# Optimization experiments

Hardware: AMD Instinct MI355X
Metric: run time of the kernel (lower is better)

The kernel has to match this reference:

```python
import jax, jax.numpy as jnp
import numpy as np

EPS = 1e-5  # BatchNorm eps


def _spmm(x, src, dst, dinv, n):
    # normalized adjacency SpMM: out[d] = dinv[d] * sum_{(s,d) in E} dinv[s] * x[s]
    msg = x[src] * dinv[src][:, None]                      # [E, d]
    agg = jax.ops.segment_sum(msg, dst, num_segments=n)   # [N, d]
    return agg * dinv[:, None]


def _cheb(x, W, b, src, dst, dinv, n):
    # Chebyshev recursion with lambda_max=2: Lhat = -Ahat
    # T0 = X, T1 = Lhat X, Tk = 2 Lhat T_{k-1} - T_{k-2}; out = sum_k T_k W_k + b
    X0 = x
    X1 = -_spmm(x, src, dst, dinv, n)
    out = X0 @ W[0] + X1 @ W[1]
    Xp, Xc = X0, X1
    for k in range(2, W.shape[0]):
        Xn = -2.0 * _spmm(Xc, src, dst, dinv, n) - Xp
        out = out + Xn @ W[k]
        Xp, Xc = Xc, Xn
    return out + b


def _bn(x, gamma, beta):
    # BatchNorm1d over nodes (training-mode batch stats)
    mu = jnp.mean(x, axis=0)
    var = jnp.var(x, axis=0)
    return (x - mu) * jax.lax.rsqrt(var + EPS) * gamma + beta


def setup_inputs() -> dict:
    key = jax.random.key(0)
    ks = jax.random.split(key, 8)
    n, e, fin, h, fout, K = 50000, 800000, 128, 128, 64, 3
    def w(k, shape, fan_in):
        return jax.random.normal(k, shape, jnp.float32) * np.float32(1.0 / np.sqrt(fan_in))
    return {
        "features": jax.random.normal(ks[0], (n, fin), jnp.float32),
        "src": jax.random.randint(ks[1], (e,), 0, n),
        "dst": jax.random.randint(ks[2], (e,), 0, n),
        "W1": w(ks[3], (K, fin, h), K * fin), "b1": jnp.zeros((h,), jnp.float32),
        "W2": w(ks[4], (K, h, h), K * h), "b2": jnp.zeros((h,), jnp.float32),
        "W3": w(ks[5], (K, h, h), K * h), "b3": jnp.zeros((h,), jnp.float32),
        "gamma": jnp.ones((h,), jnp.float32), "beta": jnp.zeros((h,), jnp.float32),
        "mw1": w(ks[6], (h, h), h), "mb1": jnp.zeros((h,), jnp.float32),
        "mw2": w(ks[7], (h, fout), h), "mb2": jnp.zeros((fout,), jnp.float32),
    }


def reference(features, src, dst, W1, b1, W2, b2, W3, b3, gamma, beta, mw1, mb1, mw2, mb2):
    n = features.shape[0]
    deg = jax.ops.segment_sum(jnp.ones(dst.shape, features.dtype), dst, num_segments=n)
    dinv = jax.lax.rsqrt(jnp.maximum(deg, 1.0))
    x = jax.nn.relu(_cheb(features, W1, b1, src, dst, dinv, n))
    x = _bn(x, gamma, beta)
    for _ in range(1, 3):  # self.k = 3 -> cheb2 applied twice (shared weights)
        x = jax.nn.relu(_cheb(x, W2, b2, src, dst, dinv, n))
    x_res = x
    x = jax.nn.relu(_cheb(x, W3, b3, src, dst, dinv, n))
    x = x + x_res  # dropout treated as identity (eval mode)
    return jax.nn.relu(x @ mw1 + mb1) @ mw2 + mb2
```

## Files before the change

kernel.cpp:

```cpp
#include <hip/hip_runtime.h>
#include <hip/hip_bf16.h>

typedef __attribute__((ext_vector_type(4))) float f32x4;
typedef __attribute__((ext_vector_type(8))) short short8;

__device__ inline unsigned short f2bf(float f) {
    union { float f; unsigned int u; } v; v.f = f;
    unsigned int u = v.u;
    return (unsigned short)((u + 0x7fffu + ((u >> 16) & 1u)) >> 16);
}
__device__ inline float bf2f(unsigned short h) {
    union { unsigned int u; float f; } v; v.u = ((unsigned int)h) << 16; return v.f;
}
__device__ inline float bflo(unsigned int p) {
    union { unsigned int u; float f; } v; v.u = p << 16; return v.f;
}
__device__ inline float bfhi(unsigned int p) {
    union { unsigned int u; float f; } v; v.u = p & 0xffff0000u; return v.f;
}
__device__ inline unsigned int packbf(float a, float b) {
    return (unsigned int)f2bf(a) | ((unsigned int)f2bf(b) << 16);
}

#define EPT 4096


__global__ __launch_bounds__(256) void cast_k(const float* __restrict__ x, unsigned short* __restrict__ y, int n4) {
    int i = blockIdx.x * 256 + threadIdx.x;
    if (i >= n4) return;
    f32x4 v = ((const f32x4*)x)[i];
    uint2 o; o.x = packbf(v[0], v[1]); o.y = packbf(v[2], v[3]);
    ((uint2*)y)[i] = o;
}


__global__ __launch_bounds__(256) void deg_rank_k(const int* __restrict__ dst, int* __restrict__ deg,
                                                  int* __restrict__ rank, int e) {
    int i = blockIdx.x * 256 + threadIdx.x;
    if (i < e) rank[i] = atomicAdd(&deg[dst[i]], 1);
}

__global__ __launch_bounds__(256) void partial_k(const int* __restrict__ deg, int* __restrict__ part, int n) {
    __shared__ int sm[256];
    int t = threadIdx.x;
    int base = blockIdx.x * 1024 + t * 4;
    int s = 0;
#pragma unroll
    for (int j = 0; j < 4; ++j) { int idx = base + j; if (idx < n) s += deg[idx]; }
    sm[t] = s;
    __syncthreads();
    for (int off = 128; off > 0; off >>= 1) {
        if (t < off) sm[t] += sm[t + off];
        __syncthreads();
    }
    if (t == 0) part[blockIdx.x] = sm[0];
}

__global__ __launch_bounds__(256) void scanpart_k(int* __restrict__ part, int nb) {
    __shared__ int sm[256];
    int t = threadIdx.x;
    int v = (t < nb) ? part[t] : 0;
    sm[t] = v;
    __syncthreads();
    for (int off = 1; off < 256; off <<= 1) {
        int u = (t >= off) ? sm[t - off] : 0;
        __syncthreads();
        sm[t] += u;
        __syncthreads();
    }
    if (t < nb) part[t] = sm[t] - v;
}

__global__ __launch_bounds__(256) void rowptr_k(const int* __restrict__ deg, const int* __restrict__ part,
                                                int* __restrict__ rowptr, float* __restrict__ dinv, int n) {
    __shared__ int sm[256];
    int t = threadIdx.x;
    int base = blockIdx.x * 1024 + t * 4;
    int d[4]; int s = 0;
#pragma unroll
    for (int j = 0; j < 4; ++j) { int idx = base + j; d[j] = (idx < n) ? deg[idx] : 0; s += d[j]; }
    sm[t] = s;
    __syncthreads();
    for (int off = 1; off < 256; off <<= 1) {
        int u = (t >= off) ? sm[t - off] : 0;
        __syncthreads();
        sm[t] += u;
        __syncthreads();
    }
    int ex = part[blockIdx.x] + sm[t] - s;
#pragma unroll
    for (int j = 0; j < 4; ++j) {
        int idx = base + j;
        if (idx < n) {
            rowptr[idx] = ex;
            dinv[idx] = rsqrtf(fmaxf((float)d[j], 1.0f));
        }
        ex += d[j];
    }
    if (blockIdx.x == gridDim.x - 1 && t == 255) rowptr[n] = part[blockIdx.x] + sm[255];
}

__global__ __launch_bounds__(256) void scatter8r_k(const int* __restrict__ src, const int* __restrict__ dst,
                                                   const int* __restrict__ rowptr, const int* __restrict__ rank,
                                                   int* __restrict__ csrc, int e, int n, int n8) {
    int r = blockIdx.x & 7;
    int chunk = blockIdx.x >> 3;
    int base = chunk * EPT;
    int lim = base + EPT; if (lim > e) lim = e;
    int lo = r * n8;
    int hi = lo + n8; if (hi > n) hi = n;
    for (int i = base + threadIdx.x; i < lim; i += 256) {
        int d = dst[i];
        if (d >= lo && d < hi) {
            csrc[rowptr[d] + rank[i]] = src[i];
        }
    }
}


template<bool AFF>
__global__ __launch_bounds__(256) void spmm_bf_k(const unsigned short* __restrict__ x, const int* __restrict__ rowptr,
                                                 const int* __restrict__ csrc, const float* __restrict__ dinv,
                                                 const float* __restrict__ gscale, const float* __restrict__ goff,
                                                 unsigned short* __restrict__ out, int n) {
    int lane = threadIdx.x & 63;
    int wave = threadIdx.x >> 6;
    int node = blockIdx.x * 4 + wave;
    if (node >= n) return;
    int g = lane >> 4;
    int c = lane & 15;
    int beg = rowptr[node], end = rowptr[node + 1];
    float acc[8];
    float sw = 0.f;
#pragma unroll
    for (int j = 0; j < 8; ++j) acc[j] = 0.f;

    int i = beg + g;
    for (; i + 12 < end; i += 16) {
        int s0 = csrc[i], s1 = csrc[i + 4], s2 = csrc[i + 8], s3 = csrc[i + 12];
        float w0 = dinv[s0], w1 = dinv[s1], w2 = dinv[s2], w3 = dinv[s3];
        uint4 v0 = ((const uint4*)(x + (size_t)s0 * 128))[c];
        uint4 v1 = ((const uint4*)(x + (size_t)s1 * 128))[c];
        uint4 v2 = ((const uint4*)(x + (size_t)s2 * 128))[c];
        uint4 v3 = ((const uint4*)(x + (size_t)s3 * 128))[c];
        if (AFF) sw += w0 + w1 + w2 + w3;
        acc[0] += w0 * bflo(v0.x); acc[1] += w0 * bfhi(v0.x);
        acc[2] += w0 * bflo(v0.y); acc[3] += w0 * bfhi(v0.y);
        acc[4] += w0 * bflo(v0.z); acc[5] += w0 * bfhi(v0.z);
        acc[6] += w0 * bflo(v0.w); acc[7] += w0 * bfhi(v0.w);
        acc[0] += w1 * bflo(v1.x); acc[1] += w1 * bfhi(v1.x);
        acc[2] += w1 * bflo(v1.y); acc[3] += w1 * bfhi(v1.y);
        acc[4] += w1 * bflo(v1.z); acc[5] += w1 * bfhi(v1.z);
        acc[6] += w1 * bflo(v1.w); acc[7] += w1 * bfhi(v1.w);
        acc[0] += w2 * bflo(v2.x); acc[1] += w2 * bfhi(v2.x);
        acc[2] += w2 * bflo(v2.y); acc[3] += w2 * bfhi(v2.y);
        acc[4] += w2 * bflo(v2.z); acc[5] += w2 * bfhi(v2.z);
        acc[6] += w2 * bflo(v2.w); acc[7] += w2 * bfhi(v2.w);
        acc[0] += w3 * bflo(v3.x); acc[1] += w3 * bfhi(v3.x);
        acc[2] += w3 * bflo(v3.y); acc[3] += w3 * bfhi(v3.y);
        acc[4] += w3 * bflo(v3.z); acc[5] += w3 * bfhi(v3.z);
        acc[6] += w3 * bflo(v3.w); acc[7] += w3 * bfhi(v3.w);
    }
    for (; i < end; i += 4) {
        int s0 = csrc[i];
        float w0 = dinv[s0];
        uint4 v0 = ((const uint4*)(x + (size_t)s0 * 128))[c];
        if (AFF) sw += w0;
        acc[0] += w0 * bflo(v0.x); acc[1] += w0 * bfhi(v0.x);
        acc[2] += w0 * bflo(v0.y); acc[3] += w0 * bfhi(v0.y);
        acc[4] += w0 * bflo(v0.z); acc[5] += w0 * bfhi(v0.z);
        acc[6] += w0 * bflo(v0.w); acc[7] += w0 * bfhi(v0.w);
    }

#pragma unroll
    for (int j = 0; j < 8; ++j) {
        acc[j] += __shfl_xor(acc[j], 16, 64);
        acc[j] += __shfl_xor(acc[j], 32, 64);
    }
    if (AFF) {
        sw += __shfl_xor(sw, 16, 64);
        sw += __shfl_xor(sw, 32, 64);
    }

    float dd = dinv[node];
    if (g == 0) {
        if (AFF) {
            f32x4 sc0 = ((const f32x4*)(gscale + c * 8))[0];
            f32x4 sc1 = ((const f32x4*)(gscale + c * 8))[1];
            f32x4 of0 = ((const f32x4*)(goff + c * 8))[0];
            f32x4 of1 = ((const f32x4*)(goff + c * 8))[1];
#pragma unroll
            for (int j = 0; j < 4; ++j) {
                acc[j] = sc0[j] * acc[j] + of0[j] * sw;
                acc[4 + j] = sc1[j] * acc[4 + j] + of1[j] * sw;
            }
        }
        uint4 o;
        o.x = packbf(acc[0] * dd, acc[1] * dd);
        o.y = packbf(acc[2] * dd, acc[3] * dd);
        o.z = packbf(acc[4] * dd, acc[5] * dd);
        o.w = packbf(acc[6] * dd, acc[7] * dd);
        ((uint4*)(out + (size_t)node * 128))[c] = o;
    }
}


__device__ inline void pack_one(const float* __restrict__ W, unsigned short* __restrict__ out,
                                int K, int N, int cheb, int id) {
    int total = (K / 32) * (N / 16) * 64;
    if (id >= total) return;
    int lane = id & 63;
    int t2 = id >> 6;
    int nf = N / 16;
    int f = t2 % nf;
    int ks = t2 / nf;
    int col = f * 16 + (lane & 15);
    int kbase = ks * 32 + ((lane >> 4) * 8);
    for (int j = 0; j < 8; ++j) {
        int kg = kbase + j;
        float v;
        if (cheb) {
            int t = kg >> 7, kk = kg & 127;
            float w0 = W[kk * 128 + col], wb = W[16384 + kk * 128 + col], wc = W[32768 + kk * 128 + col];
            v = (t == 0) ? (w0 - wc) : (t == 1) ? (-wb) : (2.0f * wc);
        } else {
            v = W[(size_t)kg * N + col];
        }
        out[(size_t)id * 8 + j] = f2bf(v);
    }
}

__global__ __launch_bounds__(256) void pack_all_k(const float* W1, unsigned short* wp1,
                                                  const float* W2, unsigned short* wp2,
                                                  const float* W3, unsigned short* wp3,
                                                  const float* mw1, unsigned short* wpm1,
                                                  const float* mw2, unsigned short* wpm2) {
    int b = blockIdx.x, t = threadIdx.x;
    if (b < 24)       pack_one(W1, wp1, 384, 128, 1, b * 256 + t);
    else if (b < 48)  pack_one(W2, wp2, 384, 128, 1, (b - 24) * 256 + t);
    else if (b < 72)  pack_one(W3, wp3, 384, 128, 1, (b - 48) * 256 + t);
    else if (b < 80)  pack_one(mw1, wpm1, 128, 128, 0, (b - 72) * 256 + t);
    else              pack_one(mw2, wpm2, 128, 64, 0, (b - 80) * 256 + t);
}


__global__ __launch_bounds__(128) void bn_coef_k(const float* __restrict__ gsum, const float* __restrict__ gsqs,
                                                 const float* __restrict__ gamma, const float* __restrict__ beta,
                                                 float* __restrict__ gscale, float* __restrict__ goff, float inv_n) {
    int c = threadIdx.x;
    float mu = gsum[c] * inv_n;
    float var = gsqs[c] * inv_n - mu * mu;
    float sc = rsqrtf(var + 1e-5f) * gamma[c];
    gscale[c] = sc;
    goff[c] = beta[c] - mu * sc;
}


template<bool RELU, bool RES, bool STATS, bool AFFA, bool MLP>
__global__ __launch_bounds__(512, 4) void gemm_k(const unsigned short* __restrict__ s0,
                                                 const unsigned short* __restrict__ s1,
                                                 const unsigned short* __restrict__ s2,
                                                 const unsigned short* __restrict__ wp,
                                                 const float* __restrict__ bias,
                                                 const unsigned short* __restrict__ resid,
                                                 const float* __restrict__ gscale,
                                                 const float* __restrict__ goff,
                                                 float* __restrict__ gsum, float* __restrict__ gsqs,
                                                 unsigned short* __restrict__ outp,
                                                 const unsigned short* __restrict__ wpm1,
                                                 const float* __restrict__ mb1,
                                                 const unsigned short* __restrict__ wpm2,
                                                 const float* __restrict__ mb2,
                                                 float* __restrict__ outf, int n) {
    __shared__ char blds[49152];
    __shared__ char tl[MLP ? 32768 : 16];
    __shared__ float bs[STATS ? 128 : 1], bq[STATS ? 128 : 1];
    int t = threadIdx.x;
    int lane = t & 63;
    int wave = t >> 6;
    int row0 = blockIdx.x * 128;

    if (STATS && t < 128) { bs[t] = 0.f; bq[t] = 0.f; }

    int rowA = row0 + wave * 16 + (lane & 15);
    if (rowA >= n) rowA = n - 1;
    int kg = (lane >> 4) * 8;
    int colb = lane & 15;

    {
        const char* gsrc = (const char*)wp;
        int wbase = wave * 6144;
#pragma unroll
        for (int j = 0; j < 6; ++j) {
            int off = wbase + j * 1024;
            __builtin_amdgcn_global_load_lds((const unsigned int*)(gsrc + off + lane * 16),
                                             (unsigned int*)(blds + off), 16, 0, 0);
        }
    }

    short8 a[12];
#pragma unroll
    for (int ks = 0; ks < 12; ++ks) {
        const unsigned short* sp = (ks < 4) ? s0 : ((ks < 8) ? s1 : s2);
        int kk = (ks & 3) * 32 + kg;
        a[ks] = *(const short8*)(sp + (size_t)rowA * 128 + kk);
    }
    if (AFFA) {
#pragma unroll
        for (int ks = 0; ks < 4; ++ks) {
            int kk = ks * 32 + kg;
            union { unsigned short u[8]; short8 v; } af;
#pragma unroll
            for (int j = 0; j < 8; ++j) {
                float xv = bf2f((unsigned short)a[ks][j]);
                af.u[j] = f2bf(xv * gscale[kk + j] + goff[kk + j]);
            }
            a[ks] = af.v;
        }
    }
#pragma unroll
    for (int ks = 0; ks < 12; ++ks) {
        f32x4 kv = *(f32x4*)&a[ks];
        asm volatile("" :: "v"(kv));
    }

    f32x4 acc[8];
#pragma unroll
    for (int f = 0; f < 8; ++f) acc[f] = (f32x4)(0.0f);

#pragma unroll
    for (int half = 0; half < 2; ++half) {
        __syncthreads();

#pragma unroll
        for (int ks6 = 0; ks6 < 6; ++ks6) {
            int ks = half * 6 + ks6;
#pragma unroll
            for (int f = 0; f < 8; ++f) {
                short8 bb = *(const short8*)(blds + (ks6 * 8 + f) * 1024 + lane * 16);
                acc[f] = __builtin_amdgcn_mfma_f32_16x16x32_bf16(a[ks], bb, acc[f], 0, 0, 0);
            }
        }

        if (half == 0) {
            __syncthreads();
            const char* gsrc = (const char*)wp + 49152;
            int wbase = wave * 6144;
#pragma unroll
            for (int j = 0; j < 6; ++j) {
                int off = wbase + j * 1024;
                __builtin_amdgcn_global_load_lds((const unsigned int*)(gsrc + off + lane * 16),
                                                 (unsigned int*)(blds + off), 16, 0, 0);
            }
        }
    }

    int rowD = row0 + wave * 16 + ((lane >> 4) << 2);
    int lrowD = wave * 16 + ((lane >> 4) << 2);
#pragma unroll
    for (int f = 0; f < 8; ++f) {
        int c = f * 16 + colb;
        float bv = bias[c];
        float ls = 0.f, lq = 0.f;
#pragma unroll
        for (int r = 0; r < 4; ++r) {
            int row = rowD + r;
            if (row >= n) continue;
            float v = acc[f][r] + bv;
            if (RELU) v = fmaxf(v, 0.0f);
            if (RES) v += bf2f(resid[(size_t)row * 128 + c]);
            if (STATS) { ls += v; lq += v * v; }
            if (MLP) {
                int lrow = lrowD + r;
                int byte = lrow * 256 + c * 2;
                byte ^= ((lrow & 7) << 4);
                *(unsigned short*)(tl + byte) = f2bf(v);
            } else {
                outp[(size_t)row * 128 + c] = f2bf(v);
            }
        }
        if (STATS) { atomicAdd(&bs[c], ls); atomicAdd(&bq[c], lq); }
    }

    if (STATS) {
        __syncthreads();
        if (t < 128) {
            atomicAdd(&gsum[t], bs[t]);
            atomicAdd(&gsqs[t], bq[t]);
        }
    }

    if (MLP) {
        __syncthreads();
        {
            int wbase = wave * 6144;
#pragma unroll
            for (int j = 0; j < 6; ++j) {
                int off = wbase + j * 1024;
                const char* g = (off < 32768) ? ((const char*)wpm1 + off)
                                              : ((const char*)wpm2 + (off - 32768));
                __builtin_amdgcn_global_load_lds((const unsigned int*)(g + lane * 16),
                                                 (unsigned int*)(blds + off), 16, 0, 0);
            }
        }
        __syncthreads();

        int lrowA = wave * 16 + (lane & 15);
        f32x4 acc2[8];
#pragma unroll
        for (int f = 0; f < 8; ++f) acc2[f] = (f32x4)(0.0f);
#pragma unroll
        for (int ks = 0; ks < 4; ++ks) {
            int byte = lrowA * 256 + (ks * 32 + kg) * 2;
            byte ^= ((lrowA & 7) << 4);
            short8 av = *(const short8*)(tl + byte);
#pragma unroll
            for (int f = 0; f < 8; ++f) {
                short8 b = *(const short8*)(blds + (ks * 8 + f) * 1024 + lane * 16);
                acc2[f] = __builtin_amdgcn_mfma_f32_16x16x32_bf16(av, b, acc2[f], 0, 0, 0);
            }
        }
        __syncthreads();

#pragma unroll
        for (int f = 0; f < 8; ++f) {
            int c = f * 16 + colb;
            float bv = mb1[c];
#pragma unroll
            for (int r = 0; r < 4; ++r) {
                int lrow = lrowD + r;
                float v = fmaxf(acc2[f][r] + bv, 0.0f);
                int byte = lrow * 256 + c * 2;
                byte ^= ((lrow & 7) << 4);
                *(unsigned short*)(tl + byte) = f2bf(v);
            }
        }
        __syncthreads();

        f32x4 acc3[4];
#pragma unroll
        for (int f = 0; f < 4; ++f) acc3[f] = (f32x4)(0.0f);
#pragma unroll
        for (int ks = 0; ks < 4; ++ks) {
            int byte = lrowA * 256 + (ks * 32 + kg) * 2;
            byte ^= ((lrowA & 7) << 4);
            short8 av = *(const short8*)(tl + byte);
#pragma unroll
            for (int f = 0; f < 4; ++f) {
                short8 b = *(const short8*)(blds + 32768 + (ks * 4 + f) * 1024 + lane * 16);
                acc3[f] = __builtin_amdgcn_mfma_f32_16x16x32_bf16(av, b, acc3[f], 0, 0, 0);
            }
        }
#pragma unroll
        for (int f = 0; f < 4; ++f) {
            int c = f * 16 + colb;
            float bv = mb2[c];
#pragma unroll
            for (int r = 0; r < 4; ++r) {
                int row = rowD + r;
                if (row >= n) continue;
                outf[(size_t)row * 64 + c] = acc3[f][r] + bv;
            }
        }
    }
}


extern "C" void kernel_launch(void* const* d_in, const int* in_sizes, int n_in,
                              void* d_out, int out_size, void* d_ws, size_t ws_size,
                              hipStream_t stream) {
    const float* feat  = (const float*)d_in[0];
    const int*   src   = (const int*)d_in[1];
    const int*   dst   = (const int*)d_in[2];
    const float* W1    = (const float*)d_in[3];
    const float* b1    = (const float*)d_in[4];
    const float* W2    = (const float*)d_in[5];
    const float* b2    = (const float*)d_in[6];
    const float* W3    = (const float*)d_in[7];
    const float* b3    = (const float*)d_in[8];
    const float* gamma = (const float*)d_in[9];
    const float* beta  = (const float*)d_in[10];
    const float* mw1   = (const float*)d_in[11];
    const float* mb1   = (const float*)d_in[12];
    const float* mw2   = (const float*)d_in[13];
    const float* mb2   = (const float*)d_in[14];
    float* outp = (float*)d_out;

    const int n = in_sizes[0] / 128;
    const int e = in_sizes[1];
    const int n8 = (n + 7) / 8;

    char* w = (char*)d_ws;
    auto alloc = [&](size_t bytes) -> void* {
        void* p = (void*)w;
        w += (bytes + 255) & ~(size_t)255;
        return p;
    };
    unsigned short* featb = (unsigned short*)alloc((size_t)n * 128 * 2);
    unsigned short* buf0  = (unsigned short*)alloc((size_t)n * 128 * 2);
    unsigned short* buf1  = (unsigned short*)alloc((size_t)n * 128 * 2);
    unsigned short* buf2  = (unsigned short*)alloc((size_t)n * 128 * 2);
    unsigned short* buf3  = (unsigned short*)alloc((size_t)n * 128 * 2);
    int*   deg    = (int*)alloc((size_t)n * 4);
    float* dinv   = (float*)alloc((size_t)n * 4);
    int*   rowptr = (int*)alloc((size_t)(n + 1) * 4);
    int*   rank   = (int*)alloc((size_t)e * 4);
    int*   csrc   = (int*)alloc((size_t)e * 4);
    int*   part   = (int*)alloc(256 * 4);
    unsigned short* wp1  = (unsigned short*)alloc(12 * 8 * 512 * 2);
    unsigned short* wp2  = (unsigned short*)alloc(12 * 8 * 512 * 2);
    unsigned short* wp3  = (unsigned short*)alloc(12 * 8 * 512 * 2);
    unsigned short* wpm1 = (unsigned short*)alloc(4 * 8 * 512 * 2);
    unsigned short* wpm2 = (unsigned short*)alloc(4 * 4 * 512 * 2);
    float* gsum   = (float*)alloc(128 * 4);
    float* gsqs   = (float*)alloc(128 * 4);
    float* gscale = (float*)alloc(128 * 4);
    float* goff   = (float*)alloc(128 * 4);

    const int gGemm = (n + 127) / 128;
    const int gSpmm = (n + 3) / 4;
    const int nb = (n + 1023) / 1024;
    const int gE  = (e + 255) / 256;
    const int gE8 = 8 * ((e + EPT - 1) / EPT);

    cast_k<<<(n * 32 + 255) / 256, 256, 0, stream>>>(feat, featb, n * 32);
    hipMemsetAsync(deg, 0, (size_t)n * 4, stream);
    hipMemsetAsync(gsum, 0, 1024, stream);
    deg_rank_k<<<gE, 256, 0, stream>>>(dst, deg, rank, e);
    partial_k<<<nb, 256, 0, stream>>>(deg, part, n);
    scanpart_k<<<1, 256, 0, stream>>>(part, nb);
    rowptr_k<<<nb, 256, 0, stream>>>(deg, part, rowptr, dinv, n);
    scatter8r_k<<<gE8, 256, 0, stream>>>(src, dst, rowptr, rank, csrc, e, n, n8);
    pack_all_k<<<84, 256, 0, stream>>>(W1, wp1, W2, wp2, W3, wp3, mw1, wpm1, mw2, wpm2);

    spmm_bf_k<false><<<gSpmm, 256, 0, stream>>>(featb, rowptr, csrc, dinv, nullptr, nullptr, buf1, n);
    spmm_bf_k<false><<<gSpmm, 256, 0, stream>>>(buf1, rowptr, csrc, dinv, nullptr, nullptr, buf2, n);
    gemm_k<true, false, true, false, false><<<gGemm, 512, 0, stream>>>(
        featb, buf1, buf2, wp1, b1, nullptr, nullptr, nullptr, gsum, gsqs, buf0,
        nullptr, nullptr, nullptr, nullptr, nullptr, n);
    bn_coef_k<<<1, 128, 0, stream>>>(gsum, gsqs, gamma, beta, gscale, goff, 1.0f / (float)n);

    spmm_bf_k<true><<<gSpmm, 256, 0, stream>>>(buf0, rowptr, csrc, dinv, gscale, goff, buf1, n);
    spmm_bf_k<false><<<gSpmm, 256, 0, stream>>>(buf1, rowptr, csrc, dinv, nullptr, nullptr, buf2, n);
    gemm_k<true, false, false, true, false><<<gGemm, 512, 0, stream>>>(
        buf0, buf1, buf2, wp2, b2, nullptr, gscale, goff, nullptr, nullptr, buf3,
        nullptr, nullptr, nullptr, nullptr, nullptr, n);

    spmm_bf_k<false><<<gSpmm, 256, 0, stream>>>(buf3, rowptr, csrc, dinv, nullptr, nullptr, buf1, n);
    spmm_bf_k<false><<<gSpmm, 256, 0, stream>>>(buf1, rowptr, csrc, dinv, nullptr, nullptr, buf2, n);
    gemm_k<true, false, false, false, false><<<gGemm, 512, 0, stream>>>(
        buf3, buf1, buf2, wp2, b2, nullptr, nullptr, nullptr, nullptr, nullptr, buf0,
        nullptr, nullptr, nullptr, nullptr, nullptr, n);

    spmm_bf_k<false><<<gSpmm, 256, 0, stream>>>(buf0, rowptr, csrc, dinv, nullptr, nullptr, buf1, n);
    spmm_bf_k<false><<<gSpmm, 256, 0, stream>>>(buf1, rowptr, csrc, dinv, nullptr, nullptr, buf2, n);
    gemm_k<true, true, false, false, true><<<gGemm, 512, 0, stream>>>(
        buf0, buf1, buf2, wp3, b3, buf0, nullptr, nullptr, nullptr, nullptr, nullptr,
        wpm1, mb1, wpm2, mb2, outp, n);
}
```

Baseline: 433.8 us.

## Fuse second Chebyshev SpMM into GEMM kernel with T2 staged in LDS

The separate second SpMM launch of each Chebyshev layer is replaced by a fused spgemm kernel. In it, each block of 64 rows first gathers its neighbors' T1 rows via CSR, writes the aggregated T2 tile as bf16 into swizzled LDS, and then runs the MFMA GEMM over T0, T1 and the LDS-resident T2. This removes four kernel launches and the global write and re-read of the T2 intermediate buffer. In exchange, blocks shrink to 256 threads and 64 rows, A operands are loaded per k-step instead of kept in registers, and LDS use per block grows. The serial per-wave gather may also be latency-bound at the reduced occupancy.

```diff
diff --git a/kernel.cpp b/kernel.cpp
--- a/kernel.cpp
+++ b/kernel.cpp
@@ -257,71 +257,111 @@
 
 
 template<bool RELU, bool RES, bool STATS, bool AFFA, bool MLP>
-__global__ __launch_bounds__(512, 4) void gemm_k(const unsigned short* __restrict__ s0,
-                                                 const unsigned short* __restrict__ s1,
-                                                 const unsigned short* __restrict__ s2,
-                                                 const unsigned short* __restrict__ wp,
-                                                 const float* __restrict__ bias,
-                                                 const unsigned short* __restrict__ resid,
-                                                 const float* __restrict__ gscale,
-                                                 const float* __restrict__ goff,
-                                                 float* __restrict__ gsum, float* __restrict__ gsqs,
-                                                 unsigned short* __restrict__ outp,
-                                                 const unsigned short* __restrict__ wpm1,
-                                                 const float* __restrict__ mb1,
-                                                 const unsigned short* __restrict__ wpm2,
-                                                 const float* __restrict__ mb2,
-                                                 float* __restrict__ outf, int n) {
+__global__ __launch_bounds__(256, 4) void spgemm_k(const unsigned short* __restrict__ s0,
+                                                   const unsigned short* __restrict__ s1,
+                                                   const int* __restrict__ rowptr,
+                                                   const int* __restrict__ csrc,
+                                                   const float* __restrict__ dinv,
+                                                   const unsigned short* __restrict__ wp,
+                                                   const float* __restrict__ bias,
+                                                   const unsigned short* __restrict__ resid,
+                                                   const float* __restrict__ gscale,
+                                                   const float* __restrict__ goff,
+                                                   float* __restrict__ gsum, float* __restrict__ gsqs,
+                                                   unsigned short* __restrict__ outp,
+                                                   const unsigned short* __restrict__ wpm1,
+                                                   const float* __restrict__ mb1,
+                                                   const unsigned short* __restrict__ wpm2,
+                                                   const float* __restrict__ mb2,
+                                                   float* __restrict__ outf, int n) {
     __shared__ char blds[49152];
-    __shared__ char tl[MLP ? 32768 : 16];
+    __shared__ char t2l[16384];
     __shared__ float bs[STATS ? 128 : 1], bq[STATS ? 128 : 1];
     int t = threadIdx.x;
     int lane = t & 63;
     int wave = t >> 6;
-    int row0 = blockIdx.x * 128;
+    int row0 = blockIdx.x * 64;
 
     if (STATS && t < 128) { bs[t] = 0.f; bq[t] = 0.f; }
 
-    int rowA = row0 + wave * 16 + (lane & 15);
-    if (rowA >= n) rowA = n - 1;
     int kg = (lane >> 4) * 8;
     int colb = lane & 15;
+    int lrow = wave * 16 + (lane & 15);
+    int rowA = row0 + lrow;
+    if (rowA >= n) rowA = n - 1;
 
     {
         const char* gsrc = (const char*)wp;
-        int wbase = wave * 6144;
-#pragma unroll
-        for (int j = 0; j < 6; ++j) {
+        int wbase = wave * 12288;
+#pragma unroll
+        for (int j = 0; j < 12; ++j) {
             int off = wbase + j * 1024;
             __builtin_amdgcn_global_load_lds((const unsigned int*)(gsrc + off + lane * 16),
                                              (unsigned int*)(blds + off), 16, 0, 0);
         }
     }
 
-    short8 a[12];
-#pragma unroll
-    for (int ks = 0; ks < 12; ++ks) {
-        const unsigned short* sp = (ks < 4) ? s0 : ((ks < 8) ? s1 : s2);
-        int kk = (ks & 3) * 32 + kg;
-        a[ks] = *(const short8*)(sp + (size_t)rowA * 128 + kk);
-    }
-    if (AFFA) {
-#pragma unroll
-        for (int ks = 0; ks < 4; ++ks) {
-            int kk = ks * 32 + kg;
-            union { unsigned short u[8]; short8 v; } af;
+    {
+        int g = lane >> 4;
+        int c = lane & 15;
+        for (int k2 = 0; k2 < 16; ++k2) {
+            int lr = wave * 16 + k2;
+            int node = row0 + lr;
+            if (node >= n) node = n - 1;
+            int beg = rowptr[node], end = rowptr[node + 1];
+            float acc[8];
+#pragma unroll
+            for (int j = 0; j < 8; ++j) acc[j] = 0.f;
+            int i = beg + g;
+            for (; i + 12 < end; i += 16) {
+                int a0 = csrc[i], a1 = csrc[i + 4], a2 = csrc[i + 8], a3 = csrc[i + 12];
+                float w0 = dinv[a0], w1 = dinv[a1], w2 = dinv[a2], w3 = dinv[a3];
+                uint4 v0 = ((const uint4*)(s1 + (size_t)a0 * 128))[c];
+                uint4 v1 = ((const uint4*)(s1 + (size_t)a1 * 128))[c];
+                uint4 v2 = ((const uint4*)(s1 + (size_t)a2 * 128))[c];
+                uint4 v3 = ((const uint4*)(s1 + (size_t)a3 * 128))[c];
+                acc[0] += w0 * bflo(v0.x); acc[1] += w0 * bfhi(v0.x);
+                acc[2] += w0 * bflo(v0.y); acc[3] += w0 * bfhi(v0.y);
+                acc[4] += w0 * bflo(v0.z); acc[5] += w0 * bfhi(v0.z);
+                acc[6] += w0 * bflo(v0.w); acc[7] += w0 * bfhi(v0.w);
+                acc[0] += w1 * bflo(v1.x); acc[1] += w1 * bfhi(v1.x);
+                acc[2] += w1 * bflo(v1.y); acc[3] += w1 * bfhi(v1.y);
+                acc[4] += w1 * bflo(v1.z); acc[5] += w1 * bfhi(v1.z);
+                acc[6] += w1 * bflo(v1.w); acc[7] += w1 * bfhi(v1.w);
+                acc[0] += w2 * bflo(v2.x); acc[1] += w2 * bfhi(v2.x);
+                acc[2] += w2 * bflo(v2.y); acc[3] += w2 * bfhi(v2.y);
+                acc[4] += w2 * bflo(v2.z); acc[5] += w2 * bfhi(v2.z);
+                acc[6] += w2 * bflo(v2.w); acc[7] += w2 * bfhi(v2.w);
+                acc[0] += w3 * bflo(v3.x); acc[1] += w3 * bfhi(v3.x);
+                acc[2] += w3 * bflo(v3.y); acc[3] += w3 * bfhi(v3.y);
+                acc[4] += w3 * bflo(v3.z); acc[5] += w3 * bfhi(v3.z);
+                acc[6] += w3 * bflo(v3.w); acc[7] += w3 * bfhi(v3.w);
+            }
+            for (; i < end; i += 4) {
+                int a0 = csrc[i];
+                float w0 = dinv[a0];
+                uint4 v0 = ((const uint4*)(s1 + (size_t)a0 * 128))[c];
+                acc[0] += w0 * bflo(v0.x); acc[1] += w0 * bfhi(v0.x);
+                acc[2] += w0 * bflo(v0.y); acc[3] += w0 * bfhi(v0.y);
+                acc[4] += w0 * bflo(v0.z); acc[5] += w0 * bfhi(v0.z);
+                acc[6] += w0 * bflo(v0.w); acc[7] += w0 * bfhi(v0.w);
+            }
 #pragma unroll
             for (int j = 0; j < 8; ++j) {
-                float xv = bf2f((unsigned short)a[ks][j]);
-                af.u[j] = f2bf(xv * gscale[kk + j] + goff[kk + j]);
-            }
-            a[ks] = af.v;
-        }
-    }
-#pragma unroll
-    for (int ks = 0; ks < 12; ++ks) {
-        f32x4 kv = *(f32x4*)&a[ks];
-        asm volatile("" :: "v"(kv));
+                acc[j] += __shfl_xor(acc[j], 16, 64);
+                acc[j] += __shfl_xor(acc[j], 32, 64);
+            }
+            float dd = dinv[node];
+            if (g == 0) {
+                uint4 o;
+                o.x = packbf(acc[0] * dd, acc[1] * dd);
+                o.y = packbf(acc[2] * dd, acc[3] * dd);
+                o.z = packbf(acc[4] * dd, acc[5] * dd);
+                o.w = packbf(acc[6] * dd, acc[7] * dd);
+                int byte = (lr * 256 + c * 16) ^ ((lr & 7) << 4);
+                *(uint4*)(t2l + byte) = o;
+            }
+        }
     }
 
     f32x4 acc[8];
@@ -335,19 +375,38 @@
 #pragma unroll
         for (int ks6 = 0; ks6 < 6; ++ks6) {
             int ks = half * 6 + ks6;
+            short8 a;
+            if (ks < 4) {
+                int kk = ks * 32 + kg;
+                a = *(const short8*)(s0 + (size_t)rowA * 128 + kk);
+                if (AFFA) {
+                    union { unsigned short u[8]; short8 v; } af;
+#pragma unroll
+                    for (int j = 0; j < 8; ++j) {
+                        float xv = bf2f((unsigned short)a[j]);
+                        af.u[j] = f2bf(xv * gscale[kk + j] + goff[kk + j]);
+                    }
+                    a = af.v;
+                }
+            } else if (ks < 8) {
+                a = *(const short8*)(s1 + (size_t)rowA * 128 + (ks & 3) * 32 + kg);
+            } else {
+                int byte = (lrow * 256 + ((ks & 3) * 32 + kg) * 2) ^ ((lrow & 7) << 4);
+                a = *(const short8*)(t2l + byte);
+            }
 #pragma unroll
             for (int f = 0; f < 8; ++f) {
                 short8 bb = *(const short8*)(blds + (ks6 * 8 + f) * 1024 + lane * 16);
-                acc[f] = __builtin_amdgcn_mfma_f32_16x16x32_bf16(a[ks], bb, acc[f], 0, 0, 0);
+                acc[f] = __builtin_amdgcn_mfma_f32_16x16x32_bf16(a, bb, acc[f], 0, 0, 0);
             }
         }
 
         if (half == 0) {
             __syncthreads();
             const char* gsrc = (const char*)wp + 49152;
-            int wbase = wave * 6144;
-#pragma unroll
-            for (int j = 0; j < 6; ++j) {
+            int wbase = wave * 12288;
+#pragma unroll
+            for (int j = 0; j < 12; ++j) {
                 int off = wbase + j * 1024;
                 __builtin_amdgcn_global_load_lds((const unsigned int*)(gsrc + off + lane * 16),
                                                  (unsigned int*)(blds + off), 16, 0, 0);
@@ -371,10 +430,9 @@
             if (RES) v += bf2f(resid[(size_t)row * 128 + c]);
             if (STATS) { ls += v; lq += v * v; }
             if (MLP) {
-                int lrow = lrowD + r;
-                int byte = lrow * 256 + c * 2;
-                byte ^= ((lrow & 7) << 4);
-                *(unsigned short*)(tl + byte) = f2bf(v);
+                int lrw = lrowD + r;
+                int byte = (lrw * 256 + c * 2) ^ ((lrw & 7) << 4);
+                *(unsigned short*)(t2l + byte) = f2bf(v);
             } else {
                 outp[(size_t)row * 128 + c] = f2bf(v);
             }
@@ -393,9 +451,9 @@
     if (MLP) {
         __syncthreads();
         {
-            int wbase = wave * 6144;
-#pragma unroll
-            for (int j = 0; j < 6; ++j) {
+            int wbase = wave * 12288;
+#pragma unroll
+            for (int j = 0; j < 12; ++j) {
                 int off = wbase + j * 1024;
                 const char* g = (off < 32768) ? ((const char*)wpm1 + off)
                                               : ((const char*)wpm2 + (off - 32768));
@@ -411,9 +469,8 @@
         for (int f = 0; f < 8; ++f) acc2[f] = (f32x4)(0.0f);
 #pragma unroll
         for (int ks = 0; ks < 4; ++ks) {
-            int byte = lrowA * 256 + (ks * 32 + kg) * 2;
-            byte ^= ((lrowA & 7) << 4);
-            short8 av = *(const short8*)(tl + byte);
+            int byte = (lrowA * 256 + (ks * 32 + kg) * 2) ^ ((lrowA & 7) << 4);
+            short8 av = *(const short8*)(t2l + byte);
 #pragma unroll
             for (int f = 0; f < 8; ++f) {
                 short8 b = *(const short8*)(blds + (ks * 8 + f) * 1024 + lane * 16);
@@ -428,11 +485,10 @@
             float bv = mb1[c];
 #pragma unroll
             for (int r = 0; r < 4; ++r) {
-                int lrow = lrowD + r;
+                int lrw = lrowD + r;
                 float v = fmaxf(acc2[f][r] + bv, 0.0f);
-                int byte = lrow * 256 + c * 2;
-                byte ^= ((lrow & 7) << 4);
-                *(unsigned short*)(tl + byte) = f2bf(v);
+                int byte = (lrw * 256 + c * 2) ^ ((lrw & 7) << 4);
+                *(unsigned short*)(t2l + byte) = f2bf(v);
             }
         }
         __syncthreads();
@@ -442,9 +498,8 @@
         for (int f = 0; f < 4; ++f) acc3[f] = (f32x4)(0.0f);
 #pragma unroll
         for (int ks = 0; ks < 4; ++ks) {
-            int byte = lrowA * 256 + (ks * 32 + kg) * 2;
-            byte ^= ((lrowA & 7) << 4);
-            short8 av = *(const short8*)(tl + byte);
+            int byte = (lrowA * 256 + (ks * 32 + kg) * 2) ^ ((lrowA & 7) << 4);
+            short8 av = *(const short8*)(t2l + byte);
 #pragma unroll
             for (int f = 0; f < 4; ++f) {
                 short8 b = *(const short8*)(blds + 32768 + (ks * 4 + f) * 1024 + lane * 16);
@@ -499,7 +554,6 @@
     unsigned short* featb = (unsigned short*)alloc((size_t)n * 128 * 2);
     unsigned short* buf0  = (unsigned short*)alloc((size_t)n * 128 * 2);
     unsigned short* buf1  = (unsigned short*)alloc((size_t)n * 128 * 2);
-    unsigned short* buf2  = (unsigned short*)alloc((size_t)n * 128 * 2);
     unsigned short* buf3  = (unsigned short*)alloc((size_t)n * 128 * 2);
     int*   deg    = (int*)alloc((size_t)n * 4);
     float* dinv   = (float*)alloc((size_t)n * 4);
@@ -517,7 +571,7 @@
     float* gscale = (float*)alloc(128 * 4);
     float* goff   = (float*)alloc(128 * 4);
 
-    const int gGemm = (n + 127) / 128;
+    const int gFus = (n + 63) / 64;
     const int gSpmm = (n + 3) / 4;
     const int nb = (n + 1023) / 1024;
     const int gE  = (e + 255) / 256;
@@ -534,27 +588,23 @@
     pack_all_k<<<84, 256, 0, stream>>>(W1, wp1, W2, wp2, W3, wp3, mw1, wpm1, mw2, wpm2);
 
     spmm_bf_k<false><<<gSpmm, 256, 0, stream>>>(featb, rowptr, csrc, dinv, nullptr, nullptr, buf1, n);
-    spmm_bf_k<false><<<gSpmm, 256, 0, stream>>>(buf1, rowptr, csrc, dinv, nullptr, nullptr, buf2, n);
-    gemm_k<true, false, true, false, false><<<gGemm, 512, 0, stream>>>(
-        featb, buf1, buf2, wp1, b1, nullptr, nullptr, nullptr, gsum, gsqs, buf0,
-        nullptr, nullptr, nullptr, nullptr, nullptr, n);
+    spgemm_k<true, false, true, false, false><<<gFus, 256, 0, stream>>>(
+        featb, buf1, rowptr, csrc, dinv, wp1, b1, nullptr, nullptr, nullptr,
+        gsum, gsqs, buf0, nullptr, nullptr, nullptr, nullptr, nullptr, n);
     bn_coef_k<<<1, 128, 0, stream>>>(gsum, gsqs, gamma, beta, gscale, goff, 1.0f / (float)n);
 
     spmm_bf_k<true><<<gSpmm, 256, 0, stream>>>(buf0, rowptr, csrc, dinv, gscale, goff, buf1, n);
-    spmm_bf_k<false><<<gSpmm, 256, 0, stream>>>(buf1, rowptr, csrc, dinv, nullptr, nullptr, buf2, n);
-    gemm_k<true, false, false, true, false><<<gGemm, 512, 0, stream>>>(
-        buf0, buf1, buf2, wp2, b2, nullptr, gscale, goff, nullptr, nullptr, buf3,
-        nullptr, nullptr, nullptr, nullptr, nullptr, n);
+    spgemm_k<true, false, false, true, false><<<gFus, 256, 0, stream>>>(
+        buf0, buf1, rowptr, csrc, dinv, wp2, b2, nullptr, gscale, goff,
+        nullptr, nullptr, buf3, nullptr, nullptr, nullptr, nullptr, nullptr, n);
 
     spmm_bf_k<false><<<gSpmm, 256, 0, stream>>>(buf3, rowptr, csrc, dinv, nullptr, nullptr, buf1, n);
-    spmm_bf_k<false><<<gSpmm, 256, 0, stream>>>(buf1, rowptr, csrc, dinv, nullptr, nullptr, buf2, n);
-    gemm_k<true, false, false, false, false><<<gGemm, 512, 0, stream>>>(
-        buf3, buf1, buf2, wp2, b2, nullptr, nullptr, nullptr, nullptr, nullptr, buf0,
-        nullptr, nullptr, nullptr, nullptr, nullptr, n);
+    spgemm_k<true, false, false, false, false><<<gFus, 256, 0, stream>>>(
+        buf3, buf1, rowptr, csrc, dinv, wp2, b2, nullptr, nullptr, nullptr,
+        nullptr, nullptr, buf0, nullptr, nullptr, nullptr, nullptr, nullptr, n);
 
     spmm_bf_k<false><<<gSpmm, 256, 0, stream>>>(buf0, rowptr, csrc, dinv, nullptr, nullptr, buf1, n);
-    spmm_bf_k<false><<<gSpmm, 256, 0, stream>>>(buf1, rowptr, csrc, dinv, nullptr, nullptr, buf2, n);
-    gemm_k<true, true, false, false, true><<<gGemm, 512, 0, stream>>>(
-        buf0, buf1, buf2, wp3, b3, buf0, nullptr, nullptr, nullptr, nullptr, nullptr,
-        wpm1, mb1, wpm2, mb2, outp, n);
-}
+    spgemm_k<true, true, false, false, true><<<gFus, 256, 0, stream>>>(
+        buf0, buf1, rowptr, csrc, dinv, wp3, b3, buf0, nullptr, nullptr,
+        nullptr, nullptr, nullptr, wpm1, mb1, wpm2, mb2, outp, n);
+}
```

New measurement: 649.4 us. 1.5x slower.
